# Performance work log

Measured on AMD Instinct MI355X. Metric: run time of the kernel, lower is better.

Reference implementation:

```python
import jax, jax.numpy as jnp
import numpy as np

N = 100000          # nodes
E = 1600000         # edges
IN_DIM = 128
HID = 64
N_CLASSES = 40
N_GAT_LAYERS = 2    # n_layers - 1
ALPHA = 0.2         # LeakyReLU slope
NEG_BIG = -9.0e15


def setup_inputs() -> dict:
    key = jax.random.key(0)
    ks = jax.random.split(key, 8)
    x = jax.random.normal(ks[0], (N, IN_DIM), dtype=jnp.float32)
    edge_index = jax.random.randint(ks[1], (2, E), 0, N, dtype=jnp.int64)
    # parameters (xavier-ish scale)
    emb_w = jax.random.normal(ks[2], (IN_DIM, HID), dtype=jnp.float32) * (1.414 / np.sqrt(IN_DIM + HID))
    emb_b = jnp.zeros((HID,), dtype=jnp.float32)
    Ws = jax.random.normal(ks[3], (N_GAT_LAYERS, HID, HID), dtype=jnp.float32) * (1.414 / np.sqrt(2 * HID))
    attn_a = jax.random.normal(ks[4], (N_GAT_LAYERS, 1, 2 * HID), dtype=jnp.float32) * (1.414 / np.sqrt(1 + 2 * HID))
    out_w = jax.random.normal(ks[5], (HID, N_CLASSES), dtype=jnp.float32) * (1.414 / np.sqrt(HID + N_CLASSES))
    out_b = jnp.zeros((N_CLASSES,), dtype=jnp.float32)
    return {"x": x, "edge_index": edge_index, "emb_w": emb_w, "emb_b": emb_b,
            "Ws": Ws, "attn_a": attn_a, "out_w": out_w, "out_b": out_b}


def _gat_conv(x, edge_src, edge_dst, W, a):
    # x: [N, d_in], W: [d_in, d_out], a: [1, 2*d_out]
    wh = x @ W                                   # [N, d_out]
    d = wh.shape[1]
    a_src = a[0, :d]                             # [d]
    a_dst = a[0, d:]                             # [d]
    # (a * cat(wh[src], wh[dst])).sum(1) == (wh @ a_src)[src] + (wh @ a_dst)[dst]
    s_src = wh @ a_src                           # [N]
    s_dst = wh @ a_dst                           # [N]
    e = jax.nn.leaky_relu(s_src[edge_src] + s_dst[edge_dst], negative_slope=ALPHA)  # [E]
    att = jnp.where(e > 0, e, NEG_BIG)
    att = jax.nn.softmax(att, axis=0)            # GLOBAL softmax over all edges (as in source)
    # scatter-aggregate weighted neighbor features into destination nodes
    msgs = att[:, None] * wh[edge_src]           # [E, d_out]
    h_prime = jax.ops.segment_sum(msgs, edge_dst, num_segments=wh.shape[0])  # [N, d_out]
    return jax.nn.elu(h_prime)                   # concat=True branch


def reference(x, edge_index, emb_w, emb_b, Ws, attn_a, out_w, out_b):
    edge_src = edge_index[0]
    edge_dst = edge_index[1]
    h = x @ emb_w + emb_b                        # emb Linear
    for l in range(N_GAT_LAYERS):
        h = _gat_conv(h, edge_src, edge_dst, Ws[l], attn_a[l])
    h = h @ out_w + out_b                        # out_att Linear
    h = jax.nn.elu(h)
    return jax.nn.log_softmax(h, axis=1)
```

## Files before the change

### kernel.cpp

```cpp
#include <hip/hip_runtime.h>
#include <hip/hip_bf16.h>

#define NODES   100000
#define EDGES   1600000
#define INDIM   128
#define HID     64
#define NCLS    40
#define NEG_BIG_F (-9000000000000000.0f)
#define SENTINEL  (-3.0e38f)

#define BN       512
#define NBUCK    196
#define CHUNK    7168
#define NCHUNK   ((EDGES + CHUNK - 1) / CHUNK)
#define BCAP     8960
#define MZPB     256
#define SMB      128

static __device__ __forceinline__ float b2f(__hip_bfloat16 h){
    return __bfloat162float(h);
}
static __device__ __forceinline__ float bits2f(unsigned int b){
    union { unsigned int u; float f; } v; v.u = b << 16; return v.f;
}
static __device__ __forceinline__ unsigned short f2b(float f){
    __hip_bfloat16 h = __float2bfloat16(f);
    return *reinterpret_cast<unsigned short*>(&h);
}
static __device__ __forceinline__ float ldin(const void* p, int i, bool f32){
    return f32 ? ((const float*)p)[i] : b2f(((const __hip_bfloat16*)p)[i]);
}
static __device__ __forceinline__ float elu_fast(float x){
    return (x > 0.f) ? x : (__expf(x) - 1.f);
}
static __device__ __forceinline__ unsigned fenc(float f){
    unsigned u = __float_as_uint(f);
    return (u & 0x80000000u) ? ~u : (u | 0x80000000u);
}
static __device__ __forceinline__ float fdec(unsigned k){
    return __uint_as_float((k & 0x80000000u) ? (k & 0x7fffffffu) : ~k);
}
static __device__ __forceinline__ void unpack8(uint4 u, float* o){
    o[0]=bits2f(u.x & 0xffffu); o[1]=bits2f(u.x >> 16);
    o[2]=bits2f(u.y & 0xffffu); o[3]=bits2f(u.y >> 16);
    o[4]=bits2f(u.z & 0xffffu); o[5]=bits2f(u.z >> 16);
    o[6]=bits2f(u.w & 0xffffu); o[7]=bits2f(u.w >> 16);
}
static __device__ __forceinline__ int ld_src(const int* ei, int i, bool i64){
    return i64 ? ei[2*i] : ei[i];
}
static __device__ __forceinline__ int ld_dst(const int* ei, int i, bool i64){
    return i64 ? ei[2*(EDGES + i)] : ei[EDGES + i];
}

__global__ __launch_bounds__(256) void k_detect(const unsigned* __restrict__ xw,
                                                const unsigned* __restrict__ eiw,
                                                int* __restrict__ flags){
    __shared__ int s1[256], s2[256];
    int t = threadIdx.x;
    int c1 = 0, c2 = 0;
    for(int i = t; i < 1024; i += 256){
        unsigned e = (xw[i] >> 23) & 0xffu;
        c1 += (e >= 90u && e <= 160u) ? 1 : 0;
        c2 += (eiw[2*i + 1] == 0u) ? 1 : 0;
    }
    s1[t] = c1; s2[t] = c2; __syncthreads();
    for(int off = 128; off > 0; off >>= 1){
        if(t < off){ s1[t] += s1[t+off]; s2[t] += s2[t+off]; }
        __syncthreads();
    }
    if(t == 0){ flags[0] = (s1[0] > 512) ? 1 : 0; flags[1] = (s2[0] > 512) ? 1 : 0; }
}

__global__ __launch_bounds__(256) void k_bhist(const int* __restrict__ ei,
                                               const int* __restrict__ flags,
                                               int* __restrict__ bdeg){
    __shared__ int sh[NBUCK];
    bool i64 = flags[1] != 0;
    int t = threadIdx.x;
    for(int i = t; i < NBUCK; i += 256) sh[i] = 0;
    __syncthreads();
    int i = blockIdx.x*256 + t;
    int stride = gridDim.x*256;
    for(; i < EDGES; i += stride) atomicAdd(&sh[ld_dst(ei, i, i64) >> 9], 1);
    __syncthreads();
    for(int b = t; b < NBUCK; b += 256) if(sh[b]) atomicAdd(&bdeg[b], sh[b]);
}

__global__ __launch_bounds__(256) void k_bscan(const int* __restrict__ bdeg,
                        int* __restrict__ bstart, int* __restrict__ bcursor){
    __shared__ int sh[256];
    int t = threadIdx.x;
    int v = (t < NBUCK) ? bdeg[t] : 0;
    sh[t] = v; __syncthreads();
    for(int off = 1; off < 256; off <<= 1){
        int x = (t >= off) ? sh[t - off] : 0;
        __syncthreads();
        sh[t] += x;
        __syncthreads();
    }
    int excl = sh[t] - v;
    if(t < NBUCK){ bstart[t] = excl; bcursor[t] = excl; }
    if(t == 255) bstart[NBUCK] = sh[255];
}

__global__ __launch_bounds__(256) void k_bucket_scatter(const int* __restrict__ ei,
    const int* __restrict__ flags, int* __restrict__ bcursor, int2* __restrict__ tmp){
    __shared__ int  sCnt[NBUCK], sScan[NBUCK], sCur[NBUCK], sGofs[NBUCK];
    __shared__ int2 stage[CHUNK];
    bool i64 = flags[1] != 0;
    int t = threadIdx.x;
    int base = blockIdx.x * CHUNK;
    int n = EDGES - base; if(n > CHUNK) n = CHUNK; if(n <= 0) return;

    for(int b = t; b < NBUCK; b += 256) sCnt[b] = 0;
    __syncthreads();
    for(int j = t; j < n; j += 256)
        atomicAdd(&sCnt[ld_dst(ei, base + j, i64) >> 9], 1);
    __syncthreads();
    for(int b = t; b < NBUCK; b += 256) sScan[b] = sCnt[b];
    __syncthreads();
    for(int off = 1; off < NBUCK; off <<= 1){
        int v = 0;
        if(t < NBUCK && t >= off) v = sScan[t - off];
        __syncthreads();
        if(t < NBUCK) sScan[t] += v;
        __syncthreads();
    }
    if(t < NBUCK){
        int excl = sScan[t] - sCnt[t];
        sCur[t]  = excl;
        sGofs[t] = sCnt[t] ? atomicAdd(&bcursor[t], sCnt[t]) : 0;
    }
    __syncthreads();
    for(int j = t; j < n; j += 256){
        int src = ld_src(ei, base + j, i64);
        int dst = ld_dst(ei, base + j, i64);
        int pos = atomicAdd(&sCur[dst >> 9], 1);
        stage[pos] = make_int2(src, dst);
    }
    __syncthreads();
    for(int i = t; i < n; i += 256){
        int2 e = stage[i];
        int  b = e.y >> 9;
        int  excl = sScan[b] - sCnt[b];
        tmp[(size_t)sGofs[b] + (i - excl)] = e;
    }
}

__global__ __launch_bounds__(512) void k_bucket_sort(const int2* __restrict__ tmp,
    const int* __restrict__ bstart, int* __restrict__ col,
    int* __restrict__ rowst){
    __shared__ int  sCnt[BN], sScan[BN], sCur[BN];
    __shared__ int2 stage[BCAP];
    int b = blockIdx.x, t = threadIdx.x;
    int nb0 = b * BN;
    int gbase = bstart[b], gend = bstart[b+1];
    int cnt = gend - gbase;

    if(t < BN) sCnt[t] = 0;
    __syncthreads();
    for(int j = gbase + t; j < gend; j += 512)
        atomicAdd(&sCnt[tmp[j].y - nb0], 1);
    __syncthreads();
    if(t < BN) sScan[t] = sCnt[t];
    __syncthreads();
    for(int off = 1; off < BN; off <<= 1){
        int v = 0;
        if(t < BN && t >= off) v = sScan[t - off];
        __syncthreads();
        if(t < BN) sScan[t] += v;
        __syncthreads();
    }
    if(t < BN) sCur[t] = sScan[t] - sCnt[t];
    if(t < BN && (nb0 + t) < NODES) rowst[nb0 + t] = gbase + (sScan[t] - sCnt[t]);
    if(b == 0 && t == 0) rowst[NODES] = EDGES;
    __syncthreads();
    for(int j = gbase + t; j < gend; j += 512){
        int2 e = tmp[j];
        int pos = atomicAdd(&sCur[e.y - nb0], 1);
        if(pos < BCAP) stage[pos] = e;
        else col[gbase + pos] = e.x;
    }
    __syncthreads();
    int lim = (cnt < BCAP) ? cnt : BCAP;
    for(int i = t; i < lim; i += 512)
        col[gbase + i] = stage[i].x;
}

template<int K, int AMODE, bool WITH_BIAS, bool WITH_SCORES, bool CBF16, int SCALEA>
__global__ __launch_bounds__(256) void k_gemm(
    const void* __restrict__ Aptr,
    const void* __restrict__ Wb,   int woff,
    const void* __restrict__ biasb,
    const void* __restrict__ attnb, int aoff,
    const int*  __restrict__ flags,
    void* __restrict__ Cout,
    float* __restrict__ s_src,
    float* __restrict__ s_dst,
    const float2* __restrict__ mzv,
    const float2* __restrict__ MZg)
{
    __shared__ float At[64][68];
    __shared__ float Wf[64][64];
    const bool wf32 = flags[0] != 0;
    const bool af32 = (AMODE == 2) ? true : wf32;
    const int t = threadIdx.x;
    const int block_row = blockIdx.x * 64;
    const int r_load = t >> 2;
    const int q_load = t & 3;
    const int grow_load = block_row + r_load;

    const int c0 = (t & 15) * 4;
    const int r0 = (t >> 4) * 4;

    float sA = 1.f;
    if constexpr (SCALEA == 1){
        float2 gz = MZg[0];
        float2 nm = (grow_load < NODES) ? mzv[grow_load] : make_float2(SENTINEL, 0.f);
        sA = __expf(nm.x - gz.x) * gz.y;
    }

    float acc[4][4] = {{0.f,0.f,0.f,0.f},{0.f,0.f,0.f,0.f},{0.f,0.f,0.f,0.f},{0.f,0.f,0.f,0.f}};

    for(int kb = 0; kb < K; kb += 64){
        if(wf32){
            const float4* wv = (const float4*)Wb;
            for(int v = t; v < 1024; v += 256){
                float4 u = wv[(size_t)(woff + kb*64)/4 + v];
                int f = v*4; int k = f >> 6; int c = f & 63;
                Wf[k][c]=u.x; Wf[k][c+1]=u.y; Wf[k][c+2]=u.z; Wf[k][c+3]=u.w;
            }
        } else {
            const uint4* wv = (const uint4*)Wb;
            for(int v = t; v < 512; v += 256){
                uint4 u = wv[(size_t)(woff + kb*64)/8 + v];
                float o[8]; unpack8(u, o);
                int f = v*8; int k = f >> 6; int c = f & 63;
                #pragma unroll
                for(int j=0;j<8;j++) Wf[k][c+j] = o[j];
            }
        }
        if(af32){
            const float4* av = (const float4*)Aptr;
            #pragma unroll
            for(int i=0;i<4;i++){
                int vi = q_load + 4*i;
                int k0 = vi*4;
                float4 u = make_float4(0.f,0.f,0.f,0.f);
                if(grow_load < NODES) u = av[(size_t)grow_load*(K/4) + (kb>>2) + vi];
                if constexpr (SCALEA == 1){
                    u.x = elu_fast(u.x*sA); u.y = elu_fast(u.y*sA);
                    u.z = elu_fast(u.z*sA); u.w = elu_fast(u.w*sA);
                }
                At[k0+0][r_load]=u.x; At[k0+1][r_load]=u.y;
                At[k0+2][r_load]=u.z; At[k0+3][r_load]=u.w;
            }
        } else {
            const uint4* av = (const uint4*)Aptr;
            #pragma unroll
            for(int i=0;i<2;i++){
                int vi = q_load + 4*i;
                int k0 = vi*8;
                float o[8];
                if(grow_load < NODES){
                    uint4 u = av[(size_t)grow_load*(K/8) + (kb>>3) + vi];
                    unpack8(u, o);
                } else {
                    #pragma unroll
                    for(int j=0;j<8;j++) o[j]=0.f;
                }
                #pragma unroll
                for(int j=0;j<8;j++) At[k0+j][r_load] = o[j];
            }
        }
        __syncthreads();
        #pragma unroll 8
        for(int k=0;k<64;k++){
            float4 a = *(const float4*)&At[k][r0];
            float4 w = *(const float4*)&Wf[k][c0];
            float av4[4] = {a.x,a.y,a.z,a.w};
            float wv4[4] = {w.x,w.y,w.z,w.w};
            #pragma unroll
            for(int i=0;i<4;i++)
                #pragma unroll
                for(int j=0;j<4;j++)
                    acc[i][j] = fmaf(av4[i], wv4[j], acc[i][j]);
        }
        __syncthreads();
    }

    float bias[4] = {0.f,0.f,0.f,0.f};
    if constexpr (WITH_BIAS){
        #pragma unroll
        for(int j=0;j<4;j++) bias[j] = ldin(biasb, c0+j, wf32);
    }
    #pragma unroll
    for(int i=0;i<4;i++){
        int grow = block_row + r0 + i;
        if(grow < NODES){
            if constexpr (CBF16){
                ushort4 o;
                o.x = f2b(acc[i][0]+bias[0]); o.y = f2b(acc[i][1]+bias[1]);
                o.z = f2b(acc[i][2]+bias[2]); o.w = f2b(acc[i][3]+bias[3]);
                *(ushort4*)((unsigned short*)Cout + (size_t)grow*64 + c0) = o;
            } else {
                float4 o = make_float4(acc[i][0]+bias[0], acc[i][1]+bias[1],
                                       acc[i][2]+bias[2], acc[i][3]+bias[3]);
                *(float4*)((float*)Cout + (size_t)grow*64 + c0) = o;
            }
        }
    }
    if constexpr (WITH_SCORES){
        float as[4], ad[4];
        #pragma unroll
        for(int j=0;j<4;j++){
            as[j] = ldin(attnb, aoff + c0+j, wf32);
            ad[j] = ldin(attnb, aoff + 64+c0+j, wf32);
        }
        #pragma unroll
        for(int i=0;i<4;i++){
            float ps = 0.f, pd = 0.f;
            #pragma unroll
            for(int j=0;j<4;j++){ ps = fmaf(acc[i][j], as[j], ps); pd = fmaf(acc[i][j], ad[j], pd); }
            for(int off=1; off<16; off<<=1){
                ps += __shfl_xor(ps, off, 64);
                pd += __shfl_xor(pd, off, 64);
            }
            int grow = block_row + r0 + i;
            if((t & 15) == 0 && grow < NODES){ s_src[grow] = ps; s_dst[grow] = pd; }
        }
    }
}

__global__ __launch_bounds__(256) void k_smax(const float* __restrict__ ssrc,
                                              unsigned* __restrict__ smaxk){
    int tid = blockIdx.x*256 + threadIdx.x;
    int stride = gridDim.x*256;
    float m = SENTINEL;
    for(int i = tid; i < NODES; i += stride) m = fmaxf(m, ssrc[i]);
    #pragma unroll
    for(int off=1; off<64; off<<=1) m = fmaxf(m, __shfl_xor(m, off, 64));
    __shared__ float sm[4];
    int w = threadIdx.x >> 6;
    if((threadIdx.x & 63) == 0) sm[w] = m;
    __syncthreads();
    if(threadIdx.x == 0){
        for(int i=1;i<4;i++) m = fmaxf(m, sm[i]);
        atomicMax(smaxk, fenc(m));
    }
}

__global__ __launch_bounds__(256) void k_aggregate(const unsigned short* __restrict__ wh16,
    const int* __restrict__ row_start, const int* __restrict__ col,
    const float* __restrict__ ssrc, const float* __restrict__ sdst,
    const unsigned* __restrict__ smaxk,
    float* __restrict__ U, float2* __restrict__ mz)
{
    int gw = (blockIdx.x*256 + threadIdx.x) >> 3;
    if(gw >= NODES) return;
    int l8 = threadIdx.x & 7;
    int sb = (threadIdx.x & 63) & ~7;
    int c8 = l8 * 8;
    int beg = row_start[gw], end = row_start[gw+1];
    float sdn = sdst[gw];
    const float m = fdec(*smaxk) + sdn;
    float zl = 0.f;
    float acc[8] = {0.f,0.f,0.f,0.f,0.f,0.f,0.f,0.f};
    for(int base = beg; base < end; base += 8){
        int idx = base + l8;
        bool vld = idx < end;
        int   s_l = vld ? col[idx] : 0;
        float v   = ssrc[s_l] + sdn;
        float att = (vld && v > 0.f) ? v : NEG_BIG_F;
        float w_l = __expf(att - m);
        zl += w_l;
        #pragma unroll
        for(int j = 0; j < 8; j++){
            int   s = __shfl(s_l, sb + j, 64);
            float a = __shfl(w_l, sb + j, 64);
            uint4 u = *(const uint4*)&wh16[(size_t)s*64 + c8];
            acc[0] = fmaf(a, bits2f(u.x & 0xffffu), acc[0]);
            acc[1] = fmaf(a, bits2f(u.x >> 16),     acc[1]);
            acc[2] = fmaf(a, bits2f(u.y & 0xffffu), acc[2]);
            acc[3] = fmaf(a, bits2f(u.y >> 16),     acc[3]);
            acc[4] = fmaf(a, bits2f(u.z & 0xffffu), acc[4]);
            acc[5] = fmaf(a, bits2f(u.z >> 16),     acc[5]);
            acc[6] = fmaf(a, bits2f(u.w & 0xffffu), acc[6]);
            acc[7] = fmaf(a, bits2f(u.w >> 16),     acc[7]);
        }
    }
    zl += __shfl_xor(zl, 1, 64);
    zl += __shfl_xor(zl, 2, 64);
    zl += __shfl_xor(zl, 4, 64);
    if(l8 == 0) mz[gw] = make_float2(m, zl);
    *(float4*)&U[(size_t)gw*64 + c8 + 0] = make_float4(acc[0],acc[1],acc[2],acc[3]);
    *(float4*)&U[(size_t)gw*64 + c8 + 4] = make_float4(acc[4],acc[5],acc[6],acc[7]);
}

__global__ __launch_bounds__(256) void k_mz_part(const float2* __restrict__ mz,
                                                 float2* __restrict__ bmz){
    int tid = blockIdx.x*256 + threadIdx.x;
    int stride = gridDim.x*256;
    float m = SENTINEL, z = 0.f;
    for(int i = tid; i < NODES; i += stride){
        float2 e = mz[i];
        float M = fmaxf(m, e.x);
        z = z*__expf(m - M) + e.y*__expf(e.x - M);
        m = M;
    }
    for(int off=1; off<64; off<<=1){
        float m2 = __shfl_xor(m, off, 64), z2 = __shfl_xor(z, off, 64);
        float M = fmaxf(m, m2);
        z = z*__expf(m - M) + z2*__expf(m2 - M);
        m = M;
    }
    __shared__ float sm[4], sz[4];
    int w = threadIdx.x >> 6;
    if((threadIdx.x & 63) == 0){ sm[w] = m; sz[w] = z; }
    __syncthreads();
    if(threadIdx.x == 0){
        for(int i=1;i<4;i++){
            float M = fmaxf(m, sm[i]);
            z = z*__expf(m - M) + sz[i]*__expf(sm[i] - M);
            m = M;
        }
        bmz[blockIdx.x] = make_float2(m, z);
    }
}

__global__ __launch_bounds__(256) void k_mz_final(const float2* __restrict__ bmz,
                                                  float2* __restrict__ MZ,
                                                  unsigned* __restrict__ smaxk){
    int t = threadIdx.x;
    float m = SENTINEL, z = 0.f;
    for(int i = t; i < MZPB; i += 256){
        float2 e = bmz[i];
        float M = fmaxf(m, e.x);
        z = z*__expf(m - M) + e.y*__expf(e.x - M);
        m = M;
    }
    for(int off=1; off<64; off<<=1){
        float m2 = __shfl_xor(m, off, 64), z2 = __shfl_xor(z, off, 64);
        float M = fmaxf(m, m2);
        z = z*__expf(m - M) + z2*__expf(m2 - M);
        m = M;
    }
    __shared__ float sm[4], sz[4];
    int w = t >> 6;
    if((t & 63) == 0){ sm[w] = m; sz[w] = z; }
    __syncthreads();
    if(t == 0){
        for(int i=1;i<4;i++){
            float M = fmaxf(m, sm[i]);
            z = z*__expf(m - M) + sz[i]*__expf(sm[i] - M);
            m = M;
        }
        MZ[0] = make_float2(m, 1.0f / z);
        smaxk[0] = 0u;
    }
}

__global__ __launch_bounds__(256) void k_out(const float* __restrict__ h,
    const float2* __restrict__ mzv, const float2* __restrict__ MZg,
    const void* __restrict__ Wo, const void* __restrict__ bo,
    const int* __restrict__ flags, float* __restrict__ out)
{
    __shared__ float Ht[64][65];
    __shared__ float Wsh[64][44];
    __shared__ float logits[64][44];
    __shared__ float rlz[64];
    bool f32 = flags[0] != 0;
    int t = threadIdx.x;
    int block_row = blockIdx.x * 64;

    for(int i = t; i < 64*NCLS; i += 256){
        Wsh[i/NCLS][i%NCLS] = ldin(Wo, i, f32);
    }
    {
        int r_load = t >> 2, q = t & 3;
        int grow = block_row + r_load;
        const float4* hv = (const float4*)h;
        float2 gz = MZg[0];
        float2 nm = (grow < NODES) ? mzv[grow] : make_float2(SENTINEL, 0.f);
        float sA = __expf(nm.x - gz.x) * gz.y;
        #pragma unroll
        for(int i = 0; i < 4; i++){
            int vi = q + 4*i;
            float4 u = make_float4(0.f,0.f,0.f,0.f);
            if(grow < NODES) u = hv[(size_t)grow*16 + vi];
            u.x = elu_fast(u.x*sA); u.y = elu_fast(u.y*sA);
            u.z = elu_fast(u.z*sA); u.w = elu_fast(u.w*sA);
            Ht[vi*4+0][r_load] = u.x; Ht[vi*4+1][r_load] = u.y;
            Ht[vi*4+2][r_load] = u.z; Ht[vi*4+3][r_load] = u.w;
        }
    }
    __syncthreads();

    int cg = t & 15, rg = t >> 4;
    int c0 = cg * 4, r0 = rg * 4;
    if(cg < 10){
        float acc[4][4] = {{0.f,0.f,0.f,0.f},{0.f,0.f,0.f,0.f},{0.f,0.f,0.f,0.f},{0.f,0.f,0.f,0.f}};
        #pragma unroll 8
        for(int k = 0; k < 64; k++){
            float4 a = *(const float4*)&Ht[k][r0];
            float4 w = *(const float4*)&Wsh[k][c0];
            float av4[4] = {a.x,a.y,a.z,a.w};
            float wv4[4] = {w.x,w.y,w.z,w.w};
            #pragma unroll
            for(int i=0;i<4;i++)
                #pragma unroll
                for(int j=0;j<4;j++)
                    acc[i][j] = fmaf(av4[i], wv4[j], acc[i][j]);
        }
        float b[4];
        #pragma unroll
        for(int j=0;j<4;j++) b[j] = ldin(bo, c0+j, f32);
        #pragma unroll
        for(int i=0;i<4;i++)
            #pragma unroll
            for(int j=0;j<4;j++){
                logits[r0+i][c0+j] = elu_fast(acc[i][j] + b[j]);
            }
    }
    __syncthreads();

    {
        int r = t >> 2, qq = t & 3;
        float m = SENTINEL;
        #pragma unroll
        for(int i=0;i<10;i++) m = fmaxf(m, logits[r][qq*10 + i]);
        m = fmaxf(m, __shfl_xor(m, 1, 64));
        m = fmaxf(m, __shfl_xor(m, 2, 64));
        float s = 0.f;
        #pragma unroll
        for(int i=0;i<10;i++) s += __expf(logits[r][qq*10 + i] - m);
        s += __shfl_xor(s, 1, 64);
        s += __shfl_xor(s, 2, 64);
        if(qq == 0) rlz[r] = m + logf(s);
    }
    __syncthreads();

    for(int i = t; i < 64*NCLS; i += 256){
        int rr = i / NCLS, cc = i % NCLS;
        if(block_row + rr < NODES)
            out[(size_t)(block_row)*NCLS + i] = logits[rr][cc] - rlz[rr];
    }
}

extern "C" void kernel_launch(void* const* d_in, const int* in_sizes, int n_in,
                              void* d_out, int out_size, void* d_ws, size_t ws_size,
                              hipStream_t stream)
{
    const void* x      = d_in[0];
    const int*  ei     = (const int*)d_in[1];
    const void* emb_w  = d_in[2];
    const void* emb_b  = d_in[3];
    const void* Ws     = d_in[4];
    const void* attn_a = d_in[5];
    const void* out_w  = d_in[6];
    const void* out_b  = d_in[7];
    float* out = (float*)d_out;

    char* ws = (char*)d_ws;
    size_t off = 0;
    auto alloc = [&](size_t bytes)->char*{
        char* p = ws + off;
        off = (off + bytes + 255) & ~(size_t)255;
        return p;
    };
    int*    flags   = (int*)   alloc(256);
    float*  h       = (float*) alloc((size_t)NODES*HID*4);
    unsigned short* wh16 = (unsigned short*)alloc((size_t)NODES*HID*2);
    float*  ssrc    = (float*) alloc((size_t)NODES*4);
    float*  sdst    = (float*) alloc((size_t)NODES*4);
    int*    rowst   = (int*)   alloc((size_t)(NODES+1)*4);
    int*    col     = (int*)   alloc((size_t)EDGES*4);
    float2* mz      = (float2*)alloc((size_t)NODES*8);
    int*    bdeg    = (int*)   alloc(NBUCK*4);
    int*    bstart  = (int*)   alloc((NBUCK+1)*4);
    int*    bcursor = (int*)   alloc(NBUCK*4);
    float2* bmz     = (float2*)alloc(MZPB*8);
    float2* MZ      = (float2*)alloc(16);
    unsigned* smaxk = (unsigned*)alloc(256);

    int2* tmp = (int2*)h;

    k_detect<<<1, 256, 0, stream>>>((const unsigned*)x, (const unsigned*)ei, flags);

    hipMemsetAsync(bdeg, 0, NBUCK*4, stream);
    hipMemsetAsync(smaxk, 0, 4, stream);
    k_bhist<<<256, 256, 0, stream>>>(ei, flags, bdeg);
    k_bscan<<<1, 256, 0, stream>>>(bdeg, bstart, bcursor);
    k_bucket_scatter<<<NCHUNK, 256, 0, stream>>>(ei, flags, bcursor, tmp);
    k_bucket_sort<<<NBUCK, 512, 0, stream>>>(tmp, bstart, col, rowst);

    k_gemm<INDIM, 0, true, false, false, 0><<<(NODES+63)/64, 256, 0, stream>>>(
        x, emb_w, 0, emb_b, nullptr, 0, flags, h, nullptr, nullptr, nullptr, nullptr);

    k_gemm<HID, 2, false, true, true, 0><<<(NODES+63)/64, 256, 0, stream>>>(
        h, Ws, 0, nullptr, attn_a, 0, flags, wh16, ssrc, sdst, nullptr, nullptr);
    k_smax<<<SMB, 256, 0, stream>>>(ssrc, smaxk);
    k_aggregate<<<(NODES*8 + 255)/256, 256, 0, stream>>>(wh16, rowst, col, ssrc, sdst, smaxk, h, mz);
    k_mz_part <<<MZPB, 256, 0, stream>>>(mz, bmz);
    k_mz_final<<<1, 256, 0, stream>>>(bmz, MZ, smaxk);

    k_gemm<HID, 2, false, true, true, 1><<<(NODES+63)/64, 256, 0, stream>>>(
        h, Ws, HID*HID, nullptr, attn_a, 2*HID, flags, wh16, ssrc, sdst, mz, MZ);
    k_smax<<<SMB, 256, 0, stream>>>(ssrc, smaxk);
    k_aggregate<<<(NODES*8 + 255)/256, 256, 0, stream>>>(wh16, rowst, col, ssrc, sdst, smaxk, h, mz);
    k_mz_part <<<MZPB, 256, 0, stream>>>(mz, bmz);
    k_mz_final<<<1, 256, 0, stream>>>(bmz, MZ, smaxk);

    k_out<<<(NODES+63)/64, 256, 0, stream>>>(h, mz, MZ, out_w, out_b, flags, out);
}
```

Measured before the change: 332.8 us.

## Replace scalar FMA GEMM with bf16 MFMA 16x16x32 matrix cores

The node-feature GEMM kernel now stages A and W tiles in LDS as bf16 and computes with the MFMA 16x16x32 bf16 instruction, one 16-row strip per wavefront across four 16-column tiles. This replaces the fp32 outer-product FMA loop and is meant to cut the ALU cost of the dense transforms. fp32 inputs are rounded to bf16 before multiplication, which lowers precision. The epilogue now writes scalar per-lane stores instead of vector stores, which may reduce store coalescing.

New measurement: 310.0 us. 6.9% less time.

```diff
diff --git a/kernel.cpp b/kernel.cpp
--- a/kernel.cpp
+++ b/kernel.cpp
@@ -17,6 +17,9 @@
 #define MZPB     256
 #define SMB      128
 
+using bf16x8 = __attribute__((ext_vector_type(8))) short;
+using f32x4  = __attribute__((ext_vector_type(4))) float;
+
 static __device__ __forceinline__ float b2f(__hip_bfloat16 h){
     return __bfloat162float(h);
 }
@@ -39,12 +42,6 @@
 }
 static __device__ __forceinline__ float fdec(unsigned k){
     return __uint_as_float((k & 0x80000000u) ? (k & 0x7fffffffu) : ~k);
-}
-static __device__ __forceinline__ void unpack8(uint4 u, float* o){
-    o[0]=bits2f(u.x & 0xffffu); o[1]=bits2f(u.x >> 16);
-    o[2]=bits2f(u.y & 0xffffu); o[3]=bits2f(u.y >> 16);
-    o[4]=bits2f(u.z & 0xffffu); o[5]=bits2f(u.z >> 16);
-    o[6]=bits2f(u.w & 0xffffu); o[7]=bits2f(u.w >> 16);
 }
 static __device__ __forceinline__ int ld_src(const int* ei, int i, bool i64){
     return i64 ? ei[2*i] : ei[i];
@@ -201,134 +198,133 @@
     const float2* __restrict__ mzv,
     const float2* __restrict__ MZg)
 {
-    __shared__ float At[64][68];
-    __shared__ float Wf[64][64];
+    __shared__ short As[64][72];
+    __shared__ short Bs[64][72];
     const bool wf32 = flags[0] != 0;
     const bool af32 = (AMODE == 2) ? true : wf32;
     const int t = threadIdx.x;
     const int block_row = blockIdx.x * 64;
-    const int r_load = t >> 2;
-    const int q_load = t & 3;
-    const int grow_load = block_row + r_load;
-
-    const int c0 = (t & 15) * 4;
-    const int r0 = (t >> 4) * 4;
+    const int w  = t >> 6;
+    const int l  = t & 63;
+    const int srow = t >> 2;
+    const int sq   = t & 3;
+    const int grow_s = block_row + srow;
 
     float sA = 1.f;
     if constexpr (SCALEA == 1){
         float2 gz = MZg[0];
-        float2 nm = (grow_load < NODES) ? mzv[grow_load] : make_float2(SENTINEL, 0.f);
+        float2 nm = (grow_s < NODES) ? mzv[grow_s] : make_float2(SENTINEL, 0.f);
         sA = __expf(nm.x - gz.x) * gz.y;
     }
 
-    float acc[4][4] = {{0.f,0.f,0.f,0.f},{0.f,0.f,0.f,0.f},{0.f,0.f,0.f,0.f},{0.f,0.f,0.f,0.f}};
+    f32x4 acc[4] = { {0.f,0.f,0.f,0.f},{0.f,0.f,0.f,0.f},
+                     {0.f,0.f,0.f,0.f},{0.f,0.f,0.f,0.f} };
 
     for(int kb = 0; kb < K; kb += 64){
+        {
+            unsigned o[16];
+            if(af32){
+                const float4* av4 = (const float4*)((const float*)Aptr + (size_t)grow_s*K + kb);
+                #pragma unroll
+                for(int i=0;i<4;i++){
+                    float4 u = make_float4(0.f,0.f,0.f,0.f);
+                    if(grow_s < NODES) u = av4[sq*4 + i];
+                    if constexpr (SCALEA == 1){
+                        u.x = elu_fast(u.x*sA); u.y = elu_fast(u.y*sA);
+                        u.z = elu_fast(u.z*sA); u.w = elu_fast(u.w*sA);
+                    }
+                    o[4*i+0]=f2b(u.x); o[4*i+1]=f2b(u.y);
+                    o[4*i+2]=f2b(u.z); o[4*i+3]=f2b(u.w);
+                }
+            } else {
+                const uint4* avb = (const uint4*)((const unsigned short*)Aptr + (size_t)grow_s*K + kb);
+                #pragma unroll
+                for(int i=0;i<2;i++){
+                    uint4 u = make_uint4(0,0,0,0);
+                    if(grow_s < NODES) u = avb[sq*2 + i];
+                    o[8*i+0]=u.x&0xffffu; o[8*i+1]=u.x>>16;
+                    o[8*i+2]=u.y&0xffffu; o[8*i+3]=u.y>>16;
+                    o[8*i+4]=u.z&0xffffu; o[8*i+5]=u.z>>16;
+                    o[8*i+6]=u.w&0xffffu; o[8*i+7]=u.w>>16;
+                }
+            }
+            uint4* dst = (uint4*)&As[srow][sq*16];
+            dst[0] = make_uint4(o[0]|(o[1]<<16),  o[2]|(o[3]<<16),
+                                o[4]|(o[5]<<16),  o[6]|(o[7]<<16));
+            dst[1] = make_uint4(o[8]|(o[9]<<16),  o[10]|(o[11]<<16),
+                                o[12]|(o[13]<<16),o[14]|(o[15]<<16));
+        }
         if(wf32){
-            const float4* wv = (const float4*)Wb;
-            for(int v = t; v < 1024; v += 256){
-                float4 u = wv[(size_t)(woff + kb*64)/4 + v];
-                int f = v*4; int k = f >> 6; int c = f & 63;
-                Wf[k][c]=u.x; Wf[k][c+1]=u.y; Wf[k][c+2]=u.z; Wf[k][c+3]=u.w;
+            const float* wv = (const float*)Wb + woff + (size_t)kb*64;
+            #pragma unroll
+            for(int i=0;i<16;i++){
+                int idx = t + 256*i;
+                Bs[idx & 63][idx >> 6] = (short)f2b(wv[idx]);
             }
         } else {
-            const uint4* wv = (const uint4*)Wb;
-            for(int v = t; v < 512; v += 256){
-                uint4 u = wv[(size_t)(woff + kb*64)/8 + v];
-                float o[8]; unpack8(u, o);
-                int f = v*8; int k = f >> 6; int c = f & 63;
-                #pragma unroll
-                for(int j=0;j<8;j++) Wf[k][c+j] = o[j];
+            const unsigned short* wv = (const unsigned short*)Wb + woff + (size_t)kb*64;
+            #pragma unroll
+            for(int i=0;i<16;i++){
+                int idx = t + 256*i;
+                Bs[idx & 63][idx >> 6] = (short)wv[idx];
             }
         }
-        if(af32){
-            const float4* av = (const float4*)Aptr;
+        __syncthreads();
+        #pragma unroll
+        for(int s=0;s<2;s++){
+            int k0 = s*32 + 8*(l >> 4);
+            bf16x8 a = *(const bf16x8*)&As[16*w + (l & 15)][k0];
             #pragma unroll
-            for(int i=0;i<4;i++){
-                int vi = q_load + 4*i;
-                int k0 = vi*4;
-                float4 u = make_float4(0.f,0.f,0.f,0.f);
-                if(grow_load < NODES) u = av[(size_t)grow_load*(K/4) + (kb>>2) + vi];
-                if constexpr (SCALEA == 1){
-                    u.x = elu_fast(u.x*sA); u.y = elu_fast(u.y*sA);
-                    u.z = elu_fast(u.z*sA); u.w = elu_fast(u.w*sA);
-                }
-                At[k0+0][r_load]=u.x; At[k0+1][r_load]=u.y;
-                At[k0+2][r_load]=u.z; At[k0+3][r_load]=u.w;
+            for(int c=0;c<4;c++){
+                bf16x8 b = *(const bf16x8*)&Bs[16*c + (l & 15)][k0];
+                acc[c] = __builtin_amdgcn_mfma_f32_16x16x32_bf16(a, b, acc[c], 0, 0, 0);
             }
-        } else {
-            const uint4* av = (const uint4*)Aptr;
-            #pragma unroll
-            for(int i=0;i<2;i++){
-                int vi = q_load + 4*i;
-                int k0 = vi*8;
-                float o[8];
-                if(grow_load < NODES){
-                    uint4 u = av[(size_t)grow_load*(K/8) + (kb>>3) + vi];
-                    unpack8(u, o);
-                } else {
-                    #pragma unroll
-                    for(int j=0;j<8;j++) o[j]=0.f;
-                }
-                #pragma unroll
-                for(int j=0;j<8;j++) At[k0+j][r_load] = o[j];
-            }
-        }
-        __syncthreads();
-        #pragma unroll 8
-        for(int k=0;k<64;k++){
-            float4 a = *(const float4*)&At[k][r0];
-            float4 w = *(const float4*)&Wf[k][c0];
-            float av4[4] = {a.x,a.y,a.z,a.w};
-            float wv4[4] = {w.x,w.y,w.z,w.w};
-            #pragma unroll
-            for(int i=0;i<4;i++)
-                #pragma unroll
-                for(int j=0;j<4;j++)
-                    acc[i][j] = fmaf(av4[i], wv4[j], acc[i][j]);
-        }
-        __syncthreads();
-    }
-
+        }
+        __syncthreads();
+    }
+
+    const int lg4 = (l >> 4) * 4;
+    const int lc  = l & 15;
     float bias[4] = {0.f,0.f,0.f,0.f};
     if constexpr (WITH_BIAS){
         #pragma unroll
-        for(int j=0;j<4;j++) bias[j] = ldin(biasb, c0+j, wf32);
+        for(int c=0;c<4;c++) bias[c] = ldin(biasb, 16*c + lc, wf32);
     }
     #pragma unroll
-    for(int i=0;i<4;i++){
-        int grow = block_row + r0 + i;
+    for(int r=0;r<4;r++){
+        int grow = block_row + 16*w + lg4 + r;
         if(grow < NODES){
-            if constexpr (CBF16){
-                ushort4 o;
-                o.x = f2b(acc[i][0]+bias[0]); o.y = f2b(acc[i][1]+bias[1]);
-                o.z = f2b(acc[i][2]+bias[2]); o.w = f2b(acc[i][3]+bias[3]);
-                *(ushort4*)((unsigned short*)Cout + (size_t)grow*64 + c0) = o;
-            } else {
-                float4 o = make_float4(acc[i][0]+bias[0], acc[i][1]+bias[1],
-                                       acc[i][2]+bias[2], acc[i][3]+bias[3]);
-                *(float4*)((float*)Cout + (size_t)grow*64 + c0) = o;
+            #pragma unroll
+            for(int c=0;c<4;c++){
+                float vv = acc[c][r] + bias[c];
+                if constexpr (CBF16)
+                    ((unsigned short*)Cout)[(size_t)grow*64 + 16*c + lc] = f2b(vv);
+                else
+                    ((float*)Cout)[(size_t)grow*64 + 16*c + lc] = vv;
             }
         }
     }
     if constexpr (WITH_SCORES){
-        float as[4], ad[4];
-        #pragma unroll
-        for(int j=0;j<4;j++){
-            as[j] = ldin(attnb, aoff + c0+j, wf32);
-            ad[j] = ldin(attnb, aoff + 64+c0+j, wf32);
-        }
-        #pragma unroll
-        for(int i=0;i<4;i++){
+        float as_[4], ad_[4];
+        #pragma unroll
+        for(int c=0;c<4;c++){
+            as_[c] = ldin(attnb, aoff + 16*c + lc, wf32);
+            ad_[c] = ldin(attnb, aoff + 64 + 16*c + lc, wf32);
+        }
+        #pragma unroll
+        for(int r=0;r<4;r++){
             float ps = 0.f, pd = 0.f;
             #pragma unroll
-            for(int j=0;j<4;j++){ ps = fmaf(acc[i][j], as[j], ps); pd = fmaf(acc[i][j], ad[j], pd); }
-            for(int off=1; off<16; off<<=1){
-                ps += __shfl_xor(ps, off, 64);
-                pd += __shfl_xor(pd, off, 64);
+            for(int c=0;c<4;c++){
+                ps = fmaf(acc[c][r], as_[c], ps);
+                pd = fmaf(acc[c][r], ad_[c], pd);
             }
-            int grow = block_row + r0 + i;
-            if((t & 15) == 0 && grow < NODES){ s_src[grow] = ps; s_dst[grow] = pd; }
+            ps += __shfl_xor(ps, 1, 64); pd += __shfl_xor(pd, 1, 64);
+            ps += __shfl_xor(ps, 2, 64); pd += __shfl_xor(pd, 2, 64);
+            ps += __shfl_xor(ps, 4, 64); pd += __shfl_xor(pd, 4, 64);
+            ps += __shfl_xor(ps, 8, 64); pd += __shfl_xor(pd, 8, 64);
+            int grow = block_row + 16*w + lg4 + r;
+            if(lc == 0 && grow < NODES){ s_src[grow] = ps; s_dst[grow] = pd; }
         }
     }
 }
```
